# Kernel optimization log

Hardware: AMD Instinct MI355X
Metric: run time of the kernel (lower is better)

The kernel has to match this reference:

```python
import jax, jax.numpy as jnp
import numpy as np

B, H, W, C, NS = 4, 96, 96, 128, 2  # batch, height, width, dim, num_splits


def _layer_norm(x, g, b, eps=1e-5):
    m = x.mean(-1, keepdims=True)
    v = x.var(-1, keepdims=True)
    return (x - m) / jnp.sqrt(v + eps) * g + b


def _split_feature(x, ns):
    # [b,h,w,c] -> [b*ns*ns, h/ns, w/ns, c] (GMFlow split_feature, channel_last)
    b, h, w, c = x.shape
    return x.reshape(b, ns, h // ns, ns, w // ns, c).transpose(0, 1, 3, 2, 4, 5).reshape(b * ns * ns, h // ns, w // ns, c)


def _merge_splits(x, ns):
    bn, h, w, c = x.shape
    b = bn // (ns * ns)
    return x.reshape(b, ns, ns, h, w, c).transpose(0, 1, 3, 2, 4, 5).reshape(b, ns * h, ns * w, c)


def _shift_mask(h, w, ns):
    # standard Swin shifted-window additive mask: 0 within region, -100 across
    wh, ww = h // ns, w // ns
    sh, sw = wh // 2, ww // 2
    img = np.zeros((h, w), dtype=np.float32)
    cnt = 0
    for hs in (slice(0, -wh), slice(-wh, -sh), slice(-sh, None)):
        for wsl in (slice(0, -ww), slice(-ww, -sw), slice(-sw, None)):
            img[hs, wsl] = cnt
            cnt += 1
    win = img.reshape(ns, wh, ns, ww).transpose(0, 2, 1, 3).reshape(ns * ns, wh * ww)
    diff = win[:, None, :] - win[:, :, None]
    return jnp.asarray(np.where(diff != 0, -100.0, 0.0).astype(np.float32))


def setup_inputs():
    key = jax.random.key(0)
    ks = jax.random.split(key, 10)
    source = jax.random.normal(ks[0], (B, H * W, C), jnp.float32)
    sc = 1.0 / float(np.sqrt(C))
    return {
        "source": source,
        "target": source,  # self-attention branch: target == source
        "mask": _shift_mask(H, W, NS),
        "h": H, "w": W,
        "ln_g": 1.0 + 0.1 * jax.random.normal(ks[1], (C,), jnp.float32),
        "ln_b": 0.1 * jax.random.normal(ks[2], (C,), jnp.float32),
        "w_gq": sc * jax.random.normal(ks[3], (C, 2 * C), jnp.float32),
        "b_gq": 0.01 * jax.random.normal(ks[4], (2 * C,), jnp.float32),
        "w_kv": sc * jax.random.normal(ks[5], (C, 2 * C), jnp.float32),
        "b_kv": 0.01 * jax.random.normal(ks[6], (2 * C,), jnp.float32),
        "w_o1": sc * jax.random.normal(ks[7], (C, C), jnp.float32),
        "b_o1": 0.01 * jax.random.normal(ks[8], (C,), jnp.float32),
        "w_o2": sc * jax.random.normal(ks[9], (C, C), jnp.float32),
    }


def reference(source, target, mask, ln_g, ln_b, w_gq, b_gq, w_kv, b_kv, w_o1, b_o1, w_o2, h, w):
    # GatedAttentionUnit, nHead=1, self-attn, attn_type='swin', with_shift=True
    ns = NS
    b, seq, c = source.shape
    wh, ww = h // ns, w // ns
    sh, sw = wh // 2, ww // 2
    s = _layer_norm(source, ln_g, ln_b)
    t = _layer_norm(target, ln_g, ln_b)
    gate, Q = jnp.split(jax.nn.silu(s @ w_gq + b_gq), 2, axis=-1)
    K, V = jnp.split(jax.nn.silu(t @ w_kv + b_kv), 2, axis=-1)

    def win(x):
        x = jnp.roll(x.reshape(b, h, w, c), (-sh, -sw), axis=(1, 2))
        return _split_feature(x, ns).reshape(b * ns * ns, wh * ww, c)

    Qw, Kw, Vw = win(Q), win(K), win(V)
    # custom scaling: dim * full seq_len (not sqrt(d))
    scores = jnp.einsum('bic,bjc->bij', Qw, Kw) / (c * seq)
    scores = scores + jnp.tile(mask, (b, 1, 1))  # mask.repeat(b,1,1)
    attn = jax.nn.softmax(scores, axis=-1)
    out = jnp.einsum('bij,bjc->bic', attn, Vw).reshape(b * ns * ns, wh, ww, c)
    out = _merge_splits(out, ns)
    out = jnp.roll(out, (sh, sw), axis=(1, 2)).reshape(b, seq, c)
    out = out * gate  # multiplicative SiLU gate
    out = jax.nn.silu(out @ w_o1 + b_o1) @ w_o2
    y = out + source
    # torch's in-place += aliases both return values to out+res
    return (y, y)
```

## Files before the change

### kernel.cpp

```cpp
#include <hip/hip_runtime.h>

typedef short s8v __attribute__((ext_vector_type(8)));
typedef float f4v __attribute__((ext_vector_type(4)));

#define MFMA16(a,b,c) __builtin_amdgcn_mfma_f32_16x16x32_bf16(a,b,c,0,0,0)

#define TOK 36864
#define SEQ 9216
#define CH 128
#define WL 2304
#define ATTN_SCALE (1.0f/1179648.0f)

__device__ __forceinline__ float b2f(unsigned short u){
  union{unsigned i; float f;} c; c.i = ((unsigned)u)<<16; return c.f;
}
__device__ __forceinline__ unsigned short f2b(float f){
  union{float f; unsigned i;} c; c.f = f;
  unsigned r = c.i + 0x7fffu + ((c.i>>16)&1u);
  return (unsigned short)(r>>16);
}
__device__ __forceinline__ int wtok(int g, int pos){
  int bi = g>>2, ih = (g>>1)&1, iw = g&1;
  int rr = pos/48, ss = pos - rr*48;
  int p = ih*48 + rr, q = iw*48 + ss;
  int i = p + 24; if (i >= 96) i -= 96;
  int j = q + 24; if (j >= 96) j -= 96;
  return bi*SEQ + i*96 + j;
}

__global__ __launch_bounds__(256) void k_prep(const float* __restrict__ wgq,
    const float* __restrict__ wkv, const float* __restrict__ wo1, const float* __restrict__ wo2,
    const float* __restrict__ bgq, const float* __restrict__ bkv, const float* __restrict__ bo1,
    const float* __restrict__ lng, const float* __restrict__ lnb,
    unsigned short* __restrict__ Wt, unsigned short* __restrict__ Wt1,
    unsigned short* __restrict__ Wt2, unsigned short* __restrict__ P)
{
  int idx = blockIdx.x*256 + threadIdx.x;
  if (idx < 65536){
    int n = idx>>7, k = idx&127;
    Wt[idx] = f2b((n<256) ? wgq[k*256+n] : wkv[k*256+(n-256)]);
  } else if (idx < 81920){
    int t2 = idx-65536; int n = t2>>7, k = t2&127;
    Wt1[t2] = f2b(wo1[k*128+n]);
  } else if (idx < 98304){
    int t2 = idx-81920; int n = t2>>7, k = t2&127;
    Wt2[t2] = f2b(wo2[k*128+n]);
  } else if (idx < 99200){
    int j = idx-98304;
    float v;
    if (j<256)      v = bgq[j];
    else if (j<512) v = bkv[j-256];
    else if (j<640) v = bo1[j-512];
    else if (j<768) v = lng[j-640];
    else            v = lnb[j-768];
    P[j] = f2b(v);
  }
}

__global__ __launch_bounds__(256) void k_proj(const float* __restrict__ src,
    const unsigned short* __restrict__ Wt, const unsigned short* __restrict__ P,
    float* __restrict__ gate, unsigned short* __restrict__ Qw,
    unsigned short* __restrict__ Kw, unsigned short* __restrict__ Vb)
{
  __shared__ __align__(16) short lS[64][136];
  __shared__ __align__(16) short lW[128][128];
  const int tid = threadIdx.x;
  const int w = tid>>6, l = tid&63, l16 = l&15, quad = l>>4;
  const int m0 = blockIdx.x*64;
  const int chunk = blockIdx.y;

  {
    int row = tid>>2, lam = tid&3;
    const float* sp = src + (m0+row)*CH + lam*32;
    float v[32]; float s = 0.f, sq = 0.f;
#pragma unroll
    for (int j=0;j<32;j++){ v[j] = sp[j]; s += v[j]; sq += v[j]*v[j]; }
    s += __shfl_xor(s,1); sq += __shfl_xor(sq,1);
    s += __shfl_xor(s,2); sq += __shfl_xor(sq,2);
    float mean = s*(1.f/128.f);
    float rstd = rsqrtf(sq*(1.f/128.f) - mean*mean + 1e-5f);
#pragma unroll
    for (int j=0;j<32;j++){
      int c = lam*32 + j;
      lS[row][c] = (short)f2b((v[j]-mean)*rstd*b2f(P[640+c]) + b2f(P[768+c]));
    }
  }
  __syncthreads();

  s8v a[4];
#pragma unroll
  for (int kc=0;kc<4;kc++) a[kc] = *(const s8v*)&lS[w*16+l16][kc*32+quad*8];

  int tokv[4], gidx[4], posv[4];
#pragma unroll
  for (int r=0;r<4;r++){
    int token = m0 + w*16 + quad*4 + r;
    int bi = token / SEQ; int t = token - bi*SEQ;
    int i = t / 96; int j = t - i*96;
    int p = i - 24; if (p<0) p += 96;
    int q = j - 24; if (q<0) q += 96;
    int ihh = (p>=48); int rr = p - ihh*48;
    int iww = (q>=48); int ss = q - iww*48;
    tokv[r] = token;
    gidx[r] = bi*4 + ihh*2 + iww;
    posv[r] = rr*48 + ss;
  }

  const int kr0 = tid>>4, kc0 = (tid&15)*8;
  const int kws = ((tid&15) ^ (kr0&7))*8;
  const unsigned short* Wsrc = Wt + (chunk*256)*CH;

  for (int sc=0; sc<2; sc++){
    const unsigned short* wp = Wsrc + (sc*128 + kr0)*CH + kc0;
#pragma unroll
    for (int j=0;j<8;j++)
      *(s8v*)&lW[j*16 + kr0][kws] = *(const s8v*)(wp + j*16*CH);
    __syncthreads();

    f4v acc[8];
#pragma unroll
    for (int nt=0;nt<8;nt++){
      f4v z = {0.f,0.f,0.f,0.f}; acc[nt] = z;
#pragma unroll
      for (int kc=0;kc<4;kc++)
        acc[nt] = MFMA16(a[kc],
                         *(const s8v*)&lW[nt*16+l16][((kc*4+quad) ^ (l16&7))*8],
                         acc[nt]);
    }
#pragma unroll
    for (int nt=0;nt<8;nt++){
      int col = chunk*256 + sc*128 + nt*16 + l16;
      float bias = b2f(P[col]);
#pragma unroll
      for (int r=0;r<4;r++){
        float z = acc[nt][r] + bias;
        z = z / (1.0f + __expf(-z));
        if (col < 128){
          gate[tokv[r]*CH + col] = z;
        } else if (col < 256){
          Qw[(gidx[r]*WL + posv[r])*CH + (col-128)] = f2b(z);
        } else if (col < 384){
          Kw[(gidx[r]*WL + posv[r])*CH + (col-256)] = f2b(z);
        } else {
          Vb[tokv[r]*CH + (col-384)] = f2b(z);
        }
      }
    }
    __syncthreads();
  }
}

__global__ __launch_bounds__(256) void k_vt(const unsigned short* __restrict__ Vb,
    unsigned short* __restrict__ Vt)
{
  __shared__ short lR[64*66];
  const int tid = threadIdx.x;
  const int g = blockIdx.y;
  const int q0 = blockIdx.x*64;
  const int lane = tid&63, grp = tid>>6;
#pragma unroll 4
  for (int p=0;p<16;p++){
    int key = p*4 + grp;
    int token = wtok(g, q0+key);
    unsigned v = *(const unsigned*)(Vb + token*CH + lane*2);
    *(unsigned*)&lR[key*66 + lane*2] = v;
  }
  __syncthreads();
#pragma unroll 8
  for (int i=0;i<32;i++){
    int ch = grp*32 + i;
    Vt[g*CH*WL + ch*WL + q0 + lane] = (unsigned short)lR[lane*66 + ch];
  }
}

__global__ __launch_bounds__(256, 3) void k_attn(const unsigned short* Qw,
    const unsigned short* __restrict__ Kw, const unsigned short* __restrict__ Vt,
    unsigned short* attn)
{
  __shared__ __align__(16) short lK[64][128];
  __shared__ __align__(16) short lV[128][64];
  __shared__ __align__(16) short lP[4][16][64];
  const int tid = threadIdx.x;
  const int w = tid>>6, l = tid&63, l16 = l&15, quad = l>>4;

  const int n  = blockIdx.x;
  const int L  = (n & 7)*72 + (n >> 3);
  const int g  = L/36;
  const int q0 = (L - g*36)*64;
  const int ih = (g>>1)&1, iw = g&1;

  const unsigned short* qp = Qw + (g*WL + q0 + w*16 + l16)*CH + quad*8;
  s8v aQ[4];
#pragma unroll
  for (int kc=0;kc<4;kc++) aQ[kc] = *(const s8v*)(qp + kc*32);

  int qrl[4], qcl[4];
#pragma unroll
  for (int r=0;r<4;r++){
    int qpj = q0 + w*16 + quad*4 + r;
    int qr = qpj/48, qs = qpj - qr*48;
    qrl[r] = (qr>=24); qcl[r] = (qs>=24);
  }

  const int kr0 = tid>>4, kc0 = (tid&15)*8;
  const int vc0 = tid>>3, vp0 = (tid&7)*8;
  const int kws = ((tid&15) ^ (kr0&7))*8;
  const int vws = ((tid&7)  ^ (vc0&7))*8;
  const unsigned short* Kbase = Kw + g*WL*CH;
  const unsigned short* Vbase = Vt + g*CH*WL;
  s8v rK[4], rV[4];

#define LOAD_TILE(kk) do { \
    const unsigned short* Kg_ = Kbase + (kk)*CH; \
    const unsigned short* Vg_ = Vbase + (kk); \
    rK[0] = *(const s8v*)(Kg_ + (kr0+ 0)*CH + kc0); \
    rK[1] = *(const s8v*)(Kg_ + (kr0+16)*CH + kc0); \
    rK[2] = *(const s8v*)(Kg_ + (kr0+32)*CH + kc0); \
    rK[3] = *(const s8v*)(Kg_ + (kr0+48)*CH + kc0); \
    rV[0] = *(const s8v*)(Vg_ + (vc0+ 0)*WL + vp0); \
    rV[1] = *(const s8v*)(Vg_ + (vc0+32)*WL + vp0); \
    rV[2] = *(const s8v*)(Vg_ + (vc0+64)*WL + vp0); \
    rV[3] = *(const s8v*)(Vg_ + (vc0+96)*WL + vp0); \
  } while(0)

#define WRITE_TILE() do { \
    *(s8v*)&lK[kr0+ 0][kws] = rK[0]; \
    *(s8v*)&lK[kr0+16][kws] = rK[1]; \
    *(s8v*)&lK[kr0+32][kws] = rK[2]; \
    *(s8v*)&lK[kr0+48][kws] = rK[3]; \
    *(s8v*)&lV[vc0+ 0][vws] = rV[0]; \
    *(s8v*)&lV[vc0+32][vws] = rV[1]; \
    *(s8v*)&lV[vc0+64][vws] = rV[2]; \
    *(s8v*)&lV[vc0+96][vws] = rV[3]; \
  } while(0)

  f4v O[8];
#pragma unroll
  for (int i=0;i<8;i++){ f4v z = {0.f,0.f,0.f,0.f}; O[i] = z; }
  float lsum[4] = {0.f,0.f,0.f,0.f};

  LOAD_TILE(0);

  for (int k0=0; k0<WL; k0+=64){
    __syncthreads();
    WRITE_TILE();
    __syncthreads();
    if (k0+64 < WL) LOAD_TILE(k0+64);

    f4v S[4];
    __builtin_amdgcn_s_setprio(1);
#pragma unroll
    for (int nt=0;nt<4;nt++){
      f4v z = {0.f,0.f,0.f,0.f}; S[nt] = z;
#pragma unroll
      for (int kc=0;kc<4;kc++)
        S[nt] = MFMA16(aQ[kc],
                       *(const s8v*)&lK[nt*16+l16][((kc*4+quad) ^ (l16&7))*8],
                       S[nt]);
    }
    __builtin_amdgcn_s_setprio(0);

#pragma unroll
    for (int nt=0;nt<4;nt++){
      int key = k0 + nt*16 + l16;
      int kr = key/48, ks = key - kr*48;
      int krl = (kr>=24), kcl = (ks>=24);
#pragma unroll
      for (int r=0;r<4;r++){
        bool masked = (ih && (krl != qrl[r])) || (iw && (kcl != qcl[r]));
        float p = masked ? 0.0f : __expf(S[nt][r]*ATTN_SCALE);
        unsigned short pb = f2b(p);
        lsum[r] += b2f(pb);
        lP[w][quad*4+r][(((nt*2)+(l16>>3)) ^ ((quad*4+r)&7))*8 + (l16&7)] = (short)pb;
      }
    }
    asm volatile("s_waitcnt lgkmcnt(0)" ::: "memory");
    __builtin_amdgcn_sched_barrier(0);

    __builtin_amdgcn_s_setprio(1);
#pragma unroll
    for (int kc2=0;kc2<2;kc2++){
      s8v aP = *(const s8v*)&lP[w][l16][((kc2*4+quad) ^ (l16&7))*8];
#pragma unroll
      for (int nt=0;nt<8;nt++)
        O[nt] = MFMA16(aP,
                       *(const s8v*)&lV[nt*16+l16][((kc2*4+quad) ^ (l16&7))*8],
                       O[nt]);
    }
    __builtin_amdgcn_s_setprio(0);
  }

#undef LOAD_TILE
#undef WRITE_TILE

#pragma unroll
  for (int r=0;r<4;r++){
#pragma unroll
    for (int m=1;m<16;m<<=1) lsum[r] += __shfl_xor(lsum[r], m);
  }
  unsigned short* outp = attn + (g*WL + q0 + w*16)*CH;
#pragma unroll
  for (int nt=0;nt<8;nt++){
#pragma unroll
    for (int r=0;r<4;r++)
      outp[(quad*4+r)*CH + nt*16 + l16] = f2b(O[nt][r] / lsum[r]);
  }
}

__global__ __launch_bounds__(256) void k_out(const unsigned short* __restrict__ attn,
    const unsigned short* __restrict__ Wo1, const unsigned short* __restrict__ P,
    const unsigned short* __restrict__ Wo2, const float* __restrict__ src,
    float* out)
{
  __shared__ __align__(16) short lA[64][136];
  __shared__ __align__(16) short lU[4][16][136];
  __shared__ __align__(16) short lW[128][128];
  const int tid = threadIdx.x;
  const int w = tid>>6, l = tid&63, l16 = l&15, quad = l>>4;
  const int m0 = blockIdx.x*64;

  const int kr0 = tid>>4, kc0 = (tid&15)*8;
  const int kws = ((tid&15) ^ (kr0&7))*8;

  {
    int r_loc = tid>>2;
    int cb = (tid&3)*32;
    int token = m0 + r_loc;
    int bi = token / SEQ; int t = token - bi*SEQ;
    int i = t / 96; int j = t - i*96;
    int p = i - 24; if (p<0) p += 96;
    int q = j - 24; if (q<0) q += 96;
    int ihh = (p>=48); int rr = p - ihh*48;
    int iww = (q>=48); int ss = q - iww*48;
    int wb = (bi*4 + ihh*2 + iww)*WL + rr*48 + ss;
    const unsigned short* av = attn + wb*CH + cb;
    const float* gv = out + token*CH + cb;
#pragma unroll
    for (int u=0;u<4;u++){
      s8v a8 = *(const s8v*)(av + u*8);
      float4 g0 = *(const float4*)(gv + u*8);
      float4 g1 = *(const float4*)(gv + u*8 + 4);
      s8v o;
      o[0]=(short)f2b(b2f((unsigned short)a8[0])*g0.x);
      o[1]=(short)f2b(b2f((unsigned short)a8[1])*g0.y);
      o[2]=(short)f2b(b2f((unsigned short)a8[2])*g0.z);
      o[3]=(short)f2b(b2f((unsigned short)a8[3])*g0.w);
      o[4]=(short)f2b(b2f((unsigned short)a8[4])*g1.x);
      o[5]=(short)f2b(b2f((unsigned short)a8[5])*g1.y);
      o[6]=(short)f2b(b2f((unsigned short)a8[6])*g1.z);
      o[7]=(short)f2b(b2f((unsigned short)a8[7])*g1.w);
      *(s8v*)&lA[r_loc][cb + u*8] = o;
    }
  }
  {
    const unsigned short* wp = Wo1 + kr0*CH + kc0;
#pragma unroll
    for (int j=0;j<8;j++)
      *(s8v*)&lW[j*16 + kr0][kws] = *(const s8v*)(wp + j*16*CH);
  }
  __syncthreads();

  s8v aA[4];
#pragma unroll
  for (int kc=0;kc<4;kc++) aA[kc] = *(const s8v*)&lA[w*16+l16][kc*32+quad*8];
  f4v acc[8];
#pragma unroll
  for (int nt=0;nt<8;nt++){
    f4v z = {0.f,0.f,0.f,0.f}; acc[nt] = z;
#pragma unroll
    for (int kc=0;kc<4;kc++)
      acc[nt] = MFMA16(aA[kc],
                       *(const s8v*)&lW[nt*16+l16][((kc*4+quad) ^ (l16&7))*8],
                       acc[nt]);
  }
#pragma unroll
  for (int nt=0;nt<8;nt++){
    int col = nt*16 + l16;
    float bias = b2f(P[512+col]);
#pragma unroll
    for (int r=0;r<4;r++){
      float z = acc[nt][r] + bias;
      z = z / (1.0f + __expf(-z));
      lU[w][quad*4+r][col] = (short)f2b(z);
    }
  }
  __syncthreads();

  {
    const unsigned short* wp = Wo2 + kr0*CH + kc0;
#pragma unroll
    for (int j=0;j<8;j++)
      *(s8v*)&lW[j*16 + kr0][kws] = *(const s8v*)(wp + j*16*CH);
  }
  __syncthreads();

  s8v aU[4];
#pragma unroll
  for (int kc=0;kc<4;kc++) aU[kc] = *(const s8v*)&lU[w][l16][kc*32+quad*8];
  f4v acc2[8];
#pragma unroll
  for (int nt=0;nt<8;nt++){
    f4v z = {0.f,0.f,0.f,0.f}; acc2[nt] = z;
#pragma unroll
    for (int kc=0;kc<4;kc++)
      acc2[nt] = MFMA16(aU[kc],
                        *(const s8v*)&lW[nt*16+l16][((kc*4+quad) ^ (l16&7))*8],
                        acc2[nt]);
  }
#pragma unroll
  for (int nt=0;nt<8;nt++){
#pragma unroll
    for (int r=0;r<4;r++){
      int token = m0 + w*16 + quad*4 + r;
      int col = nt*16 + l16;
      float y = acc2[nt][r] + src[token*CH + col];
      out[token*CH + col] = y;
      out[TOK*CH + token*CH + col] = y;
    }
  }
}

extern "C" void kernel_launch(void* const* d_in, const int* in_sizes, int n_in,
                              void* d_out, int out_size, void* d_ws, size_t ws_size,
                              hipStream_t stream)
{
  const float* src = (const float*)d_in[0];
  const float* lng = (const float*)d_in[5];
  const float* lnb = (const float*)d_in[6];
  const float* wgq = (const float*)d_in[7];
  const float* bgq = (const float*)d_in[8];
  const float* wkv = (const float*)d_in[9];
  const float* bkv = (const float*)d_in[10];
  const float* wo1 = (const float*)d_in[11];
  const float* bo1 = (const float*)d_in[12];
  const float* wo2 = (const float*)d_in[13];

  char* ws = (char*)d_ws;
  unsigned short* P   = (unsigned short*)(ws);
  unsigned short* Wt  = (unsigned short*)(ws + 2048);
  unsigned short* Wt1 = (unsigned short*)(ws + 133120);
  unsigned short* Wt2 = (unsigned short*)(ws + 165888);
  unsigned short* Qw  = (unsigned short*)(ws + 198656);
  unsigned short* Kw  = (unsigned short*)(ws + 9635840);
  unsigned short* Vt  = (unsigned short*)(ws + 19073024);
  unsigned short* Vb  = (unsigned short*)(ws + 28510208);
  float* out = (float*)d_out;

  k_prep<<<dim3(388),   dim3(256), 0, stream>>>(wgq, wkv, wo1, wo2, bgq, bkv, bo1, lng, lnb,
                                                Wt, Wt1, Wt2, P);
  k_proj<<<dim3(576,2), dim3(256), 0, stream>>>(src, Wt, P, out, Qw, Kw, Vb);
  k_vt  <<<dim3(36,16), dim3(256), 0, stream>>>(Vb, Vt);
  k_attn<<<dim3(576),   dim3(256), 0, stream>>>(Qw, Kw, Vt, Qw);
  k_out <<<dim3(576),   dim3(256), 0, stream>>>(Qw, Wt1, P, Wt2, src, out);
}
```

Before: 308.2 us.

## Double-buffer K/V tiles in LDS to drop one barrier per iteration

Result: slower. 335.0 us (+8.7%).

```diff
diff --git a/kernel.cpp b/kernel.cpp
--- a/kernel.cpp
+++ b/kernel.cpp
@@ -173,12 +173,12 @@
   }
 }
 
-__global__ __launch_bounds__(256, 3) void k_attn(const unsigned short* Qw,
+__global__ __launch_bounds__(256, 2) void k_attn(const unsigned short* Qw,
     const unsigned short* __restrict__ Kw, const unsigned short* __restrict__ Vt,
     unsigned short* attn)
 {
-  __shared__ __align__(16) short lK[64][128];
-  __shared__ __align__(16) short lV[128][64];
+  __shared__ __align__(16) short lK[2][64][128];
+  __shared__ __align__(16) short lV[2][128][64];
   __shared__ __align__(16) short lP[4][16][64];
   const int tid = threadIdx.x;
   const int w = tid>>6, l = tid&63, l16 = l&15, quad = l>>4;
@@ -223,15 +223,15 @@
     rV[3] = *(const s8v*)(Vg_ + (vc0+96)*WL + vp0); \
   } while(0)
 
-#define WRITE_TILE() do { \
-    *(s8v*)&lK[kr0+ 0][kws] = rK[0]; \
-    *(s8v*)&lK[kr0+16][kws] = rK[1]; \
-    *(s8v*)&lK[kr0+32][kws] = rK[2]; \
-    *(s8v*)&lK[kr0+48][kws] = rK[3]; \
-    *(s8v*)&lV[vc0+ 0][vws] = rV[0]; \
-    *(s8v*)&lV[vc0+32][vws] = rV[1]; \
-    *(s8v*)&lV[vc0+64][vws] = rV[2]; \
-    *(s8v*)&lV[vc0+96][vws] = rV[3]; \
+#define WRITE_TILE(b) do { \
+    *(s8v*)&lK[b][kr0+ 0][kws] = rK[0]; \
+    *(s8v*)&lK[b][kr0+16][kws] = rK[1]; \
+    *(s8v*)&lK[b][kr0+32][kws] = rK[2]; \
+    *(s8v*)&lK[b][kr0+48][kws] = rK[3]; \
+    *(s8v*)&lV[b][vc0+ 0][vws] = rV[0]; \
+    *(s8v*)&lV[b][vc0+32][vws] = rV[1]; \
+    *(s8v*)&lV[b][vc0+64][vws] = rV[2]; \
+    *(s8v*)&lV[b][vc0+96][vws] = rV[3]; \
   } while(0)
 
   f4v O[8];
@@ -240,12 +240,12 @@
   float lsum[4] = {0.f,0.f,0.f,0.f};
 
   LOAD_TILE(0);
+  WRITE_TILE(0);
+  LOAD_TILE(64);
+  __syncthreads();
 
   for (int k0=0; k0<WL; k0+=64){
-    __syncthreads();
-    WRITE_TILE();
-    __syncthreads();
-    if (k0+64 < WL) LOAD_TILE(k0+64);
+    const int cur = (k0>>6)&1;
 
     f4v S[4];
     __builtin_amdgcn_s_setprio(1);
@@ -255,7 +255,7 @@
 #pragma unroll
       for (int kc=0;kc<4;kc++)
         S[nt] = MFMA16(aQ[kc],
-                       *(const s8v*)&lK[nt*16+l16][((kc*4+quad) ^ (l16&7))*8],
+                       *(const s8v*)&lK[cur][nt*16+l16][((kc*4+quad) ^ (l16&7))*8],
                        S[nt]);
     }
     __builtin_amdgcn_s_setprio(0);
@@ -284,10 +284,16 @@
 #pragma unroll
       for (int nt=0;nt<8;nt++)
         O[nt] = MFMA16(aP,
-                       *(const s8v*)&lV[nt*16+l16][((kc2*4+quad) ^ (l16&7))*8],
+                       *(const s8v*)&lV[cur][nt*16+l16][((kc2*4+quad) ^ (l16&7))*8],
                        O[nt]);
     }
     __builtin_amdgcn_s_setprio(0);
+
+    if (k0+64 < WL){
+      WRITE_TILE(cur^1);
+      if (k0+128 < WL) LOAD_TILE(k0+128);
+      __syncthreads();
+    }
   }
 
 #undef LOAD_TILE
```
